# Kernel tuning notes

Hardware: AMD Instinct MI355X
Metric: run time of the kernel (lower is better)

Reference implementation:

```python
import jax, jax.numpy as jnp
import numpy as np

N = 100000
C_IN = 128
HEADS = 4
D_HEAD = 32
E = 1600000
NEG_SLOPE = 0.2
LN_EPS = 1e-5


def setup_inputs() -> dict:
    key = jax.random.key(0)
    ks = jax.random.split(key, 8)
    x = jax.random.normal(ks[0], (N, C_IN), dtype=jnp.float32)
    edge_index = jax.random.randint(ks[1], (2, E), 0, N, dtype=jnp.int32)
    # LayerNorm affine params
    ln_gamma = jnp.ones((C_IN,), jnp.float32)
    ln_beta = jnp.zeros((C_IN,), jnp.float32)
    # GATv2 linear layers (lin_l for source/messages, lin_r for target), glorot-ish scale
    scale = 1.0 / np.sqrt(C_IN)
    W_l = jax.random.normal(ks[2], (C_IN, HEADS * D_HEAD), jnp.float32) * scale
    b_l = jnp.zeros((HEADS * D_HEAD,), jnp.float32)
    W_r = jax.random.normal(ks[3], (C_IN, HEADS * D_HEAD), jnp.float32) * scale
    b_r = jnp.zeros((HEADS * D_HEAD,), jnp.float32)
    att = jax.random.normal(ks[4], (HEADS, D_HEAD), jnp.float32) * (1.0 / np.sqrt(D_HEAD))
    bias = jnp.zeros((D_HEAD,), jnp.float32)  # concat=False -> out_channels bias
    return {"x": x, "edge_index": edge_index, "ln_gamma": ln_gamma, "ln_beta": ln_beta,
            "W_l": W_l, "b_l": b_l, "W_r": W_r, "b_r": b_r, "att": att, "bias": bias}


def reference(x, edge_index, ln_gamma, ln_beta, W_l, b_l, W_r, b_r, att, bias):
    n = x.shape[0]
    # LayerNorm + ReLU (dropout_mask=None / eval mode)
    mu = jnp.mean(x, axis=-1, keepdims=True)
    var = jnp.mean(jnp.square(x - mu), axis=-1, keepdims=True)
    xh = (x - mu) * jax.lax.rsqrt(var + LN_EPS) * ln_gamma + ln_beta
    xh = jax.nn.relu(xh)
    # add self loops
    loops = jnp.arange(n, dtype=edge_index.dtype)
    src = jnp.concatenate([edge_index[0], loops])  # message sources j
    dst = jnp.concatenate([edge_index[1], loops])  # aggregation targets i
    # GATv2: separate transforms for source and target
    x_l = (xh @ W_l + b_l).reshape(n, HEADS, D_HEAD)
    x_r = (xh @ W_r + b_r).reshape(n, HEADS, D_HEAD)
    # edge scores: e_ij = att . leaky_relu(x_l[j] + x_r[i])
    s = x_l[src] + x_r[dst]                                      # [E+N, H, Dh]
    e = jnp.einsum('ehd,hd->eh', jax.nn.leaky_relu(s, NEG_SLOPE), att)
    # segment softmax over destination node
    m = jax.ops.segment_max(e, dst, num_segments=n)              # [N, H]
    w = jnp.exp(e - m[dst])
    denom = jax.ops.segment_sum(w, dst, num_segments=n)          # [N, H]
    alpha = w / (denom[dst] + 1e-16)                             # [E+N, H]
    # scatter-aggregate messages alpha * x_l[j]
    out = jax.ops.segment_sum(alpha[:, :, None] * x_l[src], dst, num_segments=n)  # [N, H, Dh]
    # concat=False -> mean over heads, then bias
    return out.mean(axis=1) + bias
```

## Files before the change

### kernel.cpp

```cpp
#include <hip/hip_runtime.h>
#include <math.h>


typedef __bf16 bf16x8 __attribute__((ext_vector_type(8)));
typedef float f32x4 __attribute__((ext_vector_type(4)));
typedef _Float16 h2 __attribute__((ext_vector_type(2)));

#define BIN_T 4096
#define NB_MAX 1024
#define AST 136
#define HST 136

static __device__ __forceinline__ unsigned short f2bf(float f) {
  union { float f; unsigned u; } v;
  v.f = f;
  const unsigned r = v.u + 0x7fffu + ((v.u >> 16) & 1u);
  return (unsigned short)(r >> 16);
}
static __device__ __forceinline__ float bf2f(unsigned short h) {
  union { float f; unsigned u; } v;
  v.u = ((unsigned)h) << 16;
  return v.f;
}

static __device__ __forceinline__ float quad_reduce_add(float p) {
  int a = __builtin_amdgcn_mov_dpp(__builtin_bit_cast(int, p),
                                   0xB1 , 0xf, 0xf,
                                   true);
  p += __builtin_bit_cast(float, a);
  int b = __builtin_amdgcn_mov_dpp(__builtin_bit_cast(int, p),
                                   0x4E , 0xf, 0xf,
                                   true);
  p += __builtin_bit_cast(float, b);
  return p;
}

__global__ __launch_bounds__(256) void pack_w_k(
    const float* __restrict__ Wl, const float* __restrict__ Wr,
    unsigned short* __restrict__ wph, unsigned short* __restrict__ wpl) {
  const int idx = blockIdx.x * 256 + threadIdx.x;
  const int mat = idx >> 14;
  const int rem = idx & 16383;
  const int k = rem >> 7;
  const int c = rem & 127;
  const float v = (mat ? Wr : Wl)[rem];
  const unsigned short h = f2bf(v);
  const unsigned short lo = f2bf(v - bf2f(h));
  const int po = ((mat * 4 + (k >> 5)) * 128 + c) * 32 + (k & 31);
  wph[po] = h;
  wpl[po] = lo;
}

__global__ __launch_bounds__(512, 5) void ln_gemm_mfma_k(
    const float* __restrict__ x, const float* __restrict__ gamma,
    const float* __restrict__ beta,
    const unsigned short* __restrict__ wph,
    const unsigned short* __restrict__ wpl,
    const float* __restrict__ bl, const float* __restrict__ br,
    _Float16* __restrict__ xl16, _Float16* __restrict__ xr16, int n) {
  __shared__ char smem[64 * AST * 2 * 2];
  unsigned short* const ah = (unsigned short*)smem;
  unsigned short* const al = ah + 64 * AST;
  _Float16* const sth = (_Float16*)smem;

  const int t = threadIdx.x;
  const int blk = blockIdx.x * 64;

  {
    const int r = t >> 3, q = t & 7;
    const int node = blk + r;
    float4 v[4];
    float s = 0.f, s2 = 0.f;
    const float* xrow = x + (size_t)node * 128;
#pragma unroll
    for (int rep = 0; rep < 4; rep++) {
      float4 f = make_float4(0.f, 0.f, 0.f, 0.f);
      if (node < n) f = *(const float4*)(xrow + 4 * q + 32 * rep);
      v[rep] = f;
      s += f.x + f.y + f.z + f.w;
      s2 += f.x * f.x + f.y * f.y + f.z * f.z + f.w * f.w;
    }
    s += __shfl_xor(s, 1);  s += __shfl_xor(s, 2);  s += __shfl_xor(s, 4);
    s2 += __shfl_xor(s2, 1); s2 += __shfl_xor(s2, 2); s2 += __shfl_xor(s2, 4);
    const float mu = s * (1.f / 128.f);
    const float rs = rsqrtf(s2 * (1.f / 128.f) - mu * mu + 1e-5f);
#pragma unroll
    for (int rep = 0; rep < 4; rep++) {
      const int k0 = 4 * q + 32 * rep;
      const float4 g4 = *(const float4*)(gamma + k0);
      const float4 b4 = *(const float4*)(beta + k0);
      const float ev[4] = {v[rep].x, v[rep].y, v[rep].z, v[rep].w};
      const float gv[4] = {g4.x, g4.y, g4.z, g4.w};
      const float bv[4] = {b4.x, b4.y, b4.z, b4.w};
      unsigned short hs[4], ls[4];
#pragma unroll
      for (int i2 = 0; i2 < 4; i2++) {
        float xv = (ev[i2] - mu) * rs * gv[i2] + bv[i2];
        xv = fmaxf(xv, 0.f);
        const unsigned short h = f2bf(xv);
        hs[i2] = h;
        ls[i2] = f2bf(xv - bf2f(h));
      }
      *(ushort4*)(&ah[r * AST + k0]) = make_ushort4(hs[0], hs[1], hs[2], hs[3]);
      *(ushort4*)(&al[r * AST + k0]) = make_ushort4(ls[0], ls[1], ls[2], ls[3]);
    }
  }
  __syncthreads();

  const int lane = t & 63;
  const int w = t >> 6;
  const int mat = w >> 2;
  const int cbase = (w & 3) * 32;
  const int m16 = lane & 15;
  const int quad = lane >> 4;
  const float* const biasp = mat ? br : bl;

  f32x4 acc[2][4];
  float bc[2];
#pragma unroll
  for (int ct = 0; ct < 2; ct++) {
    const int c = cbase + ct * 16 + m16;
    bf16x8 Bh[4], Bl8[4];
#pragma unroll
    for (int kb = 0; kb < 4; kb++) {
      const int bo = ((mat * 4 + kb) * 128 + c) * 32 + quad * 8;
      Bh[kb]  = *(const bf16x8*)(wph + bo);
      Bl8[kb] = *(const bf16x8*)(wpl + bo);
    }
    bc[ct] = biasp[c];
#pragma unroll
    for (int rt = 0; rt < 4; rt++) {
      f32x4 a = {0.f, 0.f, 0.f, 0.f};
#pragma unroll
      for (int kb = 0; kb < 4; kb++) {
        const int ao = (rt * 16 + m16) * AST + kb * 32 + quad * 8;
        const bf16x8 Ah  = *(const bf16x8*)(ah + ao);
        const bf16x8 Al8 = *(const bf16x8*)(al + ao);
        a = __builtin_amdgcn_mfma_f32_16x16x32_bf16(Ah,  Bh[kb],  a, 0, 0, 0);
        a = __builtin_amdgcn_mfma_f32_16x16x32_bf16(Al8, Bh[kb],  a, 0, 0, 0);
        a = __builtin_amdgcn_mfma_f32_16x16x32_bf16(Ah,  Bl8[kb], a, 0, 0, 0);
      }
      acc[ct][rt] = a;
    }
  }

  unsigned short* const outs[2] = {(unsigned short*)xl16,
                                   (unsigned short*)xr16};
#pragma unroll
  for (int round = 0; round < 2; round++) {
    __syncthreads();
    if (mat == 1 - round) {
#pragma unroll
      for (int ct = 0; ct < 2; ct++)
#pragma unroll
        for (int rt = 0; rt < 4; rt++)
#pragma unroll
          for (int g = 0; g < 4; g++)
            sth[(rt * 16 + quad * 4 + g) * HST + cbase + ct * 16 + m16] =
                (_Float16)(acc[ct][rt][g] + bc[ct]);
    }
    __syncthreads();
    unsigned short* const dst = outs[1 - round];
#pragma unroll
    for (int pass = 0; pass < 2; pass++) {
      const int idx = pass * 512 + t;
      const int row = idx >> 4;
      const int c8 = (idx & 15) * 8;
      const int node = blk + row;
      if (node < n)
        *(uint4*)(dst + (size_t)node * 128 + c8) =
            *(const uint4*)((const unsigned short*)sth + row * HST + c8);
    }
  }
}

__global__ __launch_bounds__(256) void hist_lds_k(
    const int* __restrict__ dst_arr, int* __restrict__ bucket_cnt,
    int E, int NB) {
  __shared__ int h[NB_MAX];
  const int t = threadIdx.x;
  for (int b = t; b < NB; b += 256) h[b] = 0;
  __syncthreads();
  const int beg = blockIdx.x * BIN_T;
  const int end = min(beg + BIN_T, E);
  for (int j0 = beg + t * 4; j0 < end; j0 += 1024) {
    if (j0 + 4 <= end) {
      const int4 d4 = *(const int4*)(dst_arr + j0);
      atomicAdd(&h[d4.x >> 7], 1);
      atomicAdd(&h[d4.y >> 7], 1);
      atomicAdd(&h[d4.z >> 7], 1);
      atomicAdd(&h[d4.w >> 7], 1);
    } else {
      for (int j = j0; j < end; j++) atomicAdd(&h[dst_arr[j] >> 7], 1);
    }
  }
  __syncthreads();
  for (int b = t; b < NB; b += 256) {
    const int v = h[b];
    if (v) atomicAdd(&bucket_cnt[b], v);
  }
}

__global__ __launch_bounds__(1024) void bucket_scan_k(
    const int* __restrict__ bucket_cnt, int* __restrict__ bucket_edge_off,
    int* __restrict__ bucket_cur, int* __restrict__ offsets,
    int NB, int N, int M) {
  __shared__ int lds[1024];
  const int t = threadIdx.x;
  const int v = (t < NB) ? bucket_cnt[t] : 0;
  lds[t] = v;
  __syncthreads();
  for (int d = 1; d < 1024; d <<= 1) {
    int u = 0;
    if (t >= d) u = lds[t - d];
    __syncthreads();
    lds[t] += u;
    __syncthreads();
  }
  if (t < NB) {
    const int excl = lds[t] - v;
    bucket_edge_off[t] = excl;
    bucket_cur[t] = excl;
    if (t == NB - 1) bucket_edge_off[NB] = lds[t];
  }
  if (t == 0) offsets[N] = M;
}

__global__ __launch_bounds__(256) void bin2_k(
    const int* __restrict__ ei, int* __restrict__ bucket_cur,
    unsigned* __restrict__ binned, int E, int NB) {
  __shared__ int h[NB_MAX];
  __shared__ int cur[NB_MAX];
  const int t = threadIdx.x;
  for (int b = t; b < NB; b += 256) h[b] = 0;
  __syncthreads();
  const int beg = blockIdx.x * BIN_T;
  const int end = min(beg + BIN_T, E);
  for (int j0 = beg + t * 4; j0 < end; j0 += 1024) {
    if (j0 + 4 <= end) {
      const int4 d4 = *(const int4*)(ei + E + j0);
      atomicAdd(&h[d4.x >> 7], 1);
      atomicAdd(&h[d4.y >> 7], 1);
      atomicAdd(&h[d4.z >> 7], 1);
      atomicAdd(&h[d4.w >> 7], 1);
    } else {
      for (int j = j0; j < end; j++) atomicAdd(&h[ei[E + j] >> 7], 1);
    }
  }
  __syncthreads();
  for (int b = t; b < NB; b += 256) {
    const int v = h[b];
    cur[b] = v ? atomicAdd(&bucket_cur[b], v) : 0;
  }
  __syncthreads();
  for (int j0 = beg + t * 4; j0 < end; j0 += 1024) {
    if (j0 + 4 <= end) {
      const int4 s4 = *(const int4*)(ei + j0);
      const int4 d4 = *(const int4*)(ei + E + j0);
      binned[atomicAdd(&cur[d4.x >> 7], 1)] =
          (((unsigned)d4.x & 127u) << 25) | (unsigned)s4.x;
      binned[atomicAdd(&cur[d4.y >> 7], 1)] =
          (((unsigned)d4.y & 127u) << 25) | (unsigned)s4.y;
      binned[atomicAdd(&cur[d4.z >> 7], 1)] =
          (((unsigned)d4.z & 127u) << 25) | (unsigned)s4.z;
      binned[atomicAdd(&cur[d4.w >> 7], 1)] =
          (((unsigned)d4.w & 127u) << 25) | (unsigned)s4.w;
    } else {
      for (int j = j0; j < end; j++) {
        const int s = ei[j], d = ei[E + j];
        binned[atomicAdd(&cur[d >> 7], 1)] =
            (((unsigned)d & 127u) << 25) | (unsigned)s;
      }
    }
  }
}

__global__ __launch_bounds__(256) void csr_build_k(
    const unsigned* __restrict__ binned,
    const int* __restrict__ bucket_edge_off,
    int* __restrict__ csr_src, int* __restrict__ offsets, int N, int M) {
  __shared__ int s_cnt[128];
  __shared__ int s_off[128];
  __shared__ int s_cur[128];
  const int b = blockIdx.x;
  const int t = threadIdx.x;
  if (b == 0 && t < 16) csr_src[M + t] = 0;
  const int eb = bucket_edge_off[b];
  const int ee = bucket_edge_off[b + 1];
  const int node0 = b << 7;
  if (t < 128) s_cnt[t] = 0;
  __syncthreads();
  for (int j = eb + t; j < ee; j += 256) {
    atomicAdd(&s_cnt[binned[j] >> 25], 1);
  }
  __syncthreads();
  int w = 0;
  if (t < 128) w = (node0 + t < N) ? (s_cnt[t] + 1) : 0;
  if (t < 128) s_off[t] = w;
  __syncthreads();
  for (int d = 1; d < 128; d <<= 1) {
    int u = 0;
    if (t < 128 && t >= d) u = s_off[t - d];
    __syncthreads();
    if (t < 128) s_off[t] += u;
    __syncthreads();
  }
  const int base = eb + node0;
  if (t < 128) {
    const int excl = s_off[t] - w;
    const int node = node0 + t;
    if (node < N) {
      offsets[node] = base + excl;
      csr_src[base + excl] = node;
      s_cur[t] = excl + 1;
    }
  }
  __syncthreads();
  for (int j = eb + t; j < ee; j += 256) {
    const unsigned e = binned[j];
    const int pos = atomicAdd(&s_cur[e >> 25], 1);
    csr_src[base + pos] = (int)(e & 0x1ffffffu);
  }
}

__global__ __launch_bounds__(256) void agg_fused_k(
    const uint4* __restrict__ xl4, const uint4* __restrict__ xr4,
    const float* __restrict__ att, const int* __restrict__ csr_src,
    const int* __restrict__ offsets, const float* __restrict__ bias,
    float* __restrict__ out, int n) {
  const int t = threadIdx.x;
  const int wid = t >> 6;
  const int lane = t & 63;
  const int u = lane & 15;
  const int g = lane >> 4;
  const int nwaves = gridDim.x * 4;

  h2 at[4];
  {
    const float4 a0 = *(const float4*)(att + u * 8);
    const float4 a1 = *(const float4*)(att + u * 8 + 4);
    at[0] = h2{(_Float16)a0.x, (_Float16)a0.y};
    at[1] = h2{(_Float16)a0.z, (_Float16)a0.w};
    at[2] = h2{(_Float16)a1.x, (_Float16)a1.y};
    at[3] = h2{(_Float16)a1.z, (_Float16)a1.w};
  }
  float4 b0, b1;
  if (lane < 4) {
    b0 = *(const float4*)(bias + lane * 8);
    b1 = *(const float4*)(bias + lane * 8 + 4);
  }

  const h2 slope = h2{(_Float16)0.2f, (_Float16)0.2f};
  const char* const xb = (const char*)xl4;
  const unsigned ub = (unsigned)u << 4;
  union U { uint4 u4; h2 h[4]; unsigned ui[4]; };

  for (int i = blockIdx.x * 4 + wid; i < n; i += nwaves) {
    const int off = offsets[i];
    const int end = offsets[i + 1];

    U xru; xru.u4 = xr4[(size_t)i * 16 + u];

    float den = 0.f;
    float acc[8] = {0.f, 0.f, 0.f, 0.f, 0.f, 0.f, 0.f, 0.f};

    uint4 rA = *(const uint4*)(xb + (((unsigned)csr_src[off + g] << 8) + ub));
    uint4 rB =
        *(const uint4*)(xb + (((unsigned)csr_src[off + 4 + g] << 8) + ub));

    for (int jb = off; jb < end; jb += 4) {
      U xv; xv.u4 = rA;
      rA = rB;
      rB = *(const uint4*)(xb + (((unsigned)csr_src[jb + 8 + g] << 8) + ub));

      float p = 0.f;
#pragma unroll
      for (int k = 0; k < 4; k++) {
        const h2 s = xv.h[k] + xru.h[k];
        const h2 l = __builtin_elementwise_max(s, s * slope);
        p = __builtin_amdgcn_fdot2(l, at[k], p, false);
      }
      p = quad_reduce_add(p);

      const float wgt = (jb + g < end) ? __expf(p) : 0.f;
      den += wgt;
#pragma unroll
      for (int k = 0; k < 4; k++) {
        asm("v_fma_mix_f32 %0, %1, %2, %0 op_sel:[0,0,0] op_sel_hi:[0,1,0]"
            : "+v"(acc[2 * k]) : "v"(wgt), "v"(xv.ui[k]));
        asm("v_fma_mix_f32 %0, %1, %2, %0 op_sel:[0,1,0] op_sel_hi:[0,1,0]"
            : "+v"(acc[2 * k + 1]) : "v"(wgt), "v"(xv.ui[k]));
      }
    }

    den += __shfl_xor(den, 16);
    den += __shfl_xor(den, 32);
#pragma unroll
    for (int m = 0; m < 8; m++) {
      acc[m] += __shfl_xor(acc[m], 16);
      acc[m] += __shfl_xor(acc[m], 32);
    }
    const float rd = 1.0f / (den + 1e-16f);
#pragma unroll
    for (int m = 0; m < 8; m++) acc[m] *= rd;
#pragma unroll
    for (int m = 0; m < 8; m++) {
      acc[m] += __shfl_xor(acc[m], 4);
      acc[m] += __shfl_xor(acc[m], 8);
    }
    if (lane < 4) {
      float4 o0 = make_float4(acc[0] * 0.25f + b0.x, acc[1] * 0.25f + b0.y,
                              acc[2] * 0.25f + b0.z, acc[3] * 0.25f + b0.w);
      float4 o1 = make_float4(acc[4] * 0.25f + b1.x, acc[5] * 0.25f + b1.y,
                              acc[6] * 0.25f + b1.z, acc[7] * 0.25f + b1.w);
      *(float4*)(out + (size_t)i * 32 + lane * 8) = o0;
      *(float4*)(out + (size_t)i * 32 + lane * 8 + 4) = o1;
    }
  }
}

extern "C" void kernel_launch(void* const* d_in, const int* in_sizes, int n_in,
                              void* d_out, int out_size, void* d_ws,
                              size_t ws_size, hipStream_t stream) {
  const float* x     = (const float*)d_in[0];
  const int*   ei    = (const int*)d_in[1];
  const float* gamma = (const float*)d_in[2];
  const float* beta  = (const float*)d_in[3];
  const float* Wl    = (const float*)d_in[4];
  const float* bl    = (const float*)d_in[5];
  const float* Wr    = (const float*)d_in[6];
  const float* br    = (const float*)d_in[7];
  const float* att   = (const float*)d_in[8];
  const float* bias  = (const float*)d_in[9];
  float* out = (float*)d_out;

  const int N = in_sizes[0] / 128;
  const int E = in_sizes[1] / 2;
  const int M = E + N;
  const int NB = (N + 127) / 128;

  char* p = (char*)d_ws;
  size_t o = 0;
  auto alloc = [&](size_t bytes) -> void* {
    void* r = (void*)(p + o);
    o = (o + bytes + 255) & ~(size_t)255;
    return r;
  };
  _Float16* xl16   = (_Float16*)alloc((size_t)N * 128 * 2);
  unsigned* binned = (unsigned*)xl16;
  _Float16* xr16 = (_Float16*)alloc((size_t)N * 128 * 2);
  int*   csr_src = (int*)alloc((size_t)M * 4 + 64);
  int*   offsets = (int*)alloc((size_t)(N + 1) * 4);
  int*   bucket_cnt = (int*)alloc((size_t)NB * 4);
  int*   bucket_off = (int*)alloc((size_t)(NB + 1) * 4);
  int*   bucket_cur = (int*)alloc((size_t)NB * 4);
  unsigned short* wph = (unsigned short*)alloc(2 * 128 * 128 * 2);
  unsigned short* wpl = (unsigned short*)alloc(2 * 128 * 128 * 2);
  (void)n_in; (void)out_size; (void)ws_size;

  const int nchunks = (E + BIN_T - 1) / BIN_T;

  hipMemsetAsync(bucket_cnt, 0, (size_t)NB * 4, stream);
  hist_lds_k<<<nchunks, 256, 0, stream>>>(ei + E, bucket_cnt, E, NB);
  bucket_scan_k<<<1, 1024, 0, stream>>>(bucket_cnt, bucket_off, bucket_cur,
                                        offsets, NB, N, M);
  bin2_k<<<nchunks, 256, 0, stream>>>(ei, bucket_cur, binned, E, NB);
  csr_build_k<<<NB, 256, 0, stream>>>(binned, bucket_off, csr_src, offsets,
                                      N, M);

  pack_w_k<<<128, 256, 0, stream>>>(Wl, Wr, wph, wpl);
  ln_gemm_mfma_k<<<(N + 63) / 64, 512, 0, stream>>>(x, gamma, beta, wph, wpl,
                                                    bl, br, xl16, xr16, N);

  const int nodeWaves = (N + 3) / 4;
  const int aggBlocks = nodeWaves < 2048 ? nodeWaves : 2048;
  agg_fused_k<<<aggBlocks, 256, 0, stream>>>((const uint4*)xl16,
                                             (const uint4*)xr16, att,
                                             csr_src, offsets, bias, out, N);
}
```

Measured before the change: 261.3 us.

## Reuse per-chunk histograms in binning, prescale CSR indices, deepen gather prefetch

The histogram kernel now writes each chunk's bucket counts to workspace, so the binning kernel no longer rereads the destination array and rebuilds its LDS histogram. The CSR source indices are stored pre-shifted by the 256-byte row stride, which removes a shift per gathered row in the aggregation loop. The aggregation loop prefetches one extra edge index ahead (three-deep row pipeline), and the attention vector is prescaled by log2(e) so the exponential can use the native exp2 instruction. The cost is extra workspace traffic for the per-chunk histograms and a few more registers for the deeper prefetch.

```diff
diff --git a/kernel.cpp b/kernel.cpp
--- a/kernel.cpp
+++ b/kernel.cpp
@@ -176,7 +176,7 @@
 
 __global__ __launch_bounds__(256) void hist_lds_k(
     const int* __restrict__ dst_arr, int* __restrict__ bucket_cnt,
-    int E, int NB) {
+    int* __restrict__ hist_chunks, int E, int NB) {
   __shared__ int h[NB_MAX];
   const int t = threadIdx.x;
   for (int b = t; b < NB; b += 256) h[b] = 0;
@@ -195,8 +195,10 @@
     }
   }
   __syncthreads();
+  int* const hc = hist_chunks + (size_t)blockIdx.x * NB;
   for (int b = t; b < NB; b += 256) {
     const int v = h[b];
+    hc[b] = v;
     if (v) atomicAdd(&bucket_cnt[b], v);
   }
 }
@@ -228,31 +230,18 @@
 
 __global__ __launch_bounds__(256) void bin2_k(
     const int* __restrict__ ei, int* __restrict__ bucket_cur,
+    const int* __restrict__ hist_chunks,
     unsigned* __restrict__ binned, int E, int NB) {
-  __shared__ int h[NB_MAX];
   __shared__ int cur[NB_MAX];
   const int t = threadIdx.x;
-  for (int b = t; b < NB; b += 256) h[b] = 0;
+  const int* const hc = hist_chunks + (size_t)blockIdx.x * NB;
+  for (int b = t; b < NB; b += 256) {
+    const int v = hc[b];
+    cur[b] = v ? atomicAdd(&bucket_cur[b], v) : 0;
+  }
   __syncthreads();
   const int beg = blockIdx.x * BIN_T;
   const int end = min(beg + BIN_T, E);
-  for (int j0 = beg + t * 4; j0 < end; j0 += 1024) {
-    if (j0 + 4 <= end) {
-      const int4 d4 = *(const int4*)(ei + E + j0);
-      atomicAdd(&h[d4.x >> 7], 1);
-      atomicAdd(&h[d4.y >> 7], 1);
-      atomicAdd(&h[d4.z >> 7], 1);
-      atomicAdd(&h[d4.w >> 7], 1);
-    } else {
-      for (int j = j0; j < end; j++) atomicAdd(&h[ei[E + j] >> 7], 1);
-    }
-  }
-  __syncthreads();
-  for (int b = t; b < NB; b += 256) {
-    const int v = h[b];
-    cur[b] = v ? atomicAdd(&bucket_cur[b], v) : 0;
-  }
-  __syncthreads();
   for (int j0 = beg + t * 4; j0 < end; j0 += 1024) {
     if (j0 + 4 <= end) {
       const int4 s4 = *(const int4*)(ei + j0);
@@ -278,7 +267,7 @@
 __global__ __launch_bounds__(256) void csr_build_k(
     const unsigned* __restrict__ binned,
     const int* __restrict__ bucket_edge_off,
-    int* __restrict__ csr_src, int* __restrict__ offsets, int N, int M) {
+    unsigned* __restrict__ csr_src, int* __restrict__ offsets, int N, int M) {
   __shared__ int s_cnt[128];
   __shared__ int s_off[128];
   __shared__ int s_cur[128];
@@ -311,7 +300,7 @@
     const int node = node0 + t;
     if (node < N) {
       offsets[node] = base + excl;
-      csr_src[base + excl] = node;
+      csr_src[base + excl] = (unsigned)node << 8;
       s_cur[t] = excl + 1;
     }
   }
@@ -319,13 +308,13 @@
   for (int j = eb + t; j < ee; j += 256) {
     const unsigned e = binned[j];
     const int pos = atomicAdd(&s_cur[e >> 25], 1);
-    csr_src[base + pos] = (int)(e & 0x1ffffffu);
+    csr_src[base + pos] = (e & 0x1ffffffu) << 8;
   }
 }
 
 __global__ __launch_bounds__(256) void agg_fused_k(
     const uint4* __restrict__ xl4, const uint4* __restrict__ xr4,
-    const float* __restrict__ att, const int* __restrict__ csr_src,
+    const float* __restrict__ att, const unsigned* __restrict__ csr_src,
     const int* __restrict__ offsets, const float* __restrict__ bias,
     float* __restrict__ out, int n) {
   const int t = threadIdx.x;
@@ -337,12 +326,13 @@
 
   h2 at[4];
   {
+    const float L2E = 1.44269504f;
     const float4 a0 = *(const float4*)(att + u * 8);
     const float4 a1 = *(const float4*)(att + u * 8 + 4);
-    at[0] = h2{(_Float16)a0.x, (_Float16)a0.y};
-    at[1] = h2{(_Float16)a0.z, (_Float16)a0.w};
-    at[2] = h2{(_Float16)a1.x, (_Float16)a1.y};
-    at[3] = h2{(_Float16)a1.z, (_Float16)a1.w};
+    at[0] = h2{(_Float16)(a0.x * L2E), (_Float16)(a0.y * L2E)};
+    at[1] = h2{(_Float16)(a0.z * L2E), (_Float16)(a0.w * L2E)};
+    at[2] = h2{(_Float16)(a1.x * L2E), (_Float16)(a1.y * L2E)};
+    at[3] = h2{(_Float16)(a1.z * L2E), (_Float16)(a1.w * L2E)};
   }
   float4 b0, b1;
   if (lane < 4) {
@@ -351,8 +341,7 @@
   }
 
   const h2 slope = h2{(_Float16)0.2f, (_Float16)0.2f};
-  const char* const xb = (const char*)xl4;
-  const unsigned ub = (unsigned)u << 4;
+  const char* const xbu = (const char*)xl4 + ((unsigned)u << 4);
   union U { uint4 u4; h2 h[4]; unsigned ui[4]; };
 
   for (int i = blockIdx.x * 4 + wid; i < n; i += nwaves) {
@@ -364,14 +353,14 @@
     float den = 0.f;
     float acc[8] = {0.f, 0.f, 0.f, 0.f, 0.f, 0.f, 0.f, 0.f};
 
-    uint4 rA = *(const uint4*)(xb + (((unsigned)csr_src[off + g] << 8) + ub));
-    uint4 rB =
-        *(const uint4*)(xb + (((unsigned)csr_src[off + 4 + g] << 8) + ub));
+    unsigned iC = csr_src[off + 8 + g];
+    uint4 rA = *(const uint4*)(xbu + csr_src[off + g]);
+    uint4 rB = *(const uint4*)(xbu + csr_src[off + 4 + g]);
 
     for (int jb = off; jb < end; jb += 4) {
       U xv; xv.u4 = rA;
-      rA = rB;
-      rB = *(const uint4*)(xb + (((unsigned)csr_src[jb + 8 + g] << 8) + ub));
+      const uint4 rC = *(const uint4*)(xbu + iC);
+      iC = csr_src[jb + 12 + g];
 
       float p = 0.f;
 #pragma unroll
@@ -382,7 +371,8 @@
       }
       p = quad_reduce_add(p);
 
-      const float wgt = (jb + g < end) ? __expf(p) : 0.f;
+      const float wgt =
+          (jb + g < end) ? __builtin_amdgcn_exp2f(p) : 0.f;
       den += wgt;
 #pragma unroll
       for (int k = 0; k < 4; k++) {
@@ -391,6 +381,8 @@
         asm("v_fma_mix_f32 %0, %1, %2, %0 op_sel:[0,1,0] op_sel_hi:[0,1,0]"
             : "+v"(acc[2 * k + 1]) : "v"(wgt), "v"(xv.ui[k]));
       }
+      rA = rB;
+      rB = rC;
     }
 
     den += __shfl_xor(den, 16);
@@ -438,6 +430,7 @@
   const int E = in_sizes[1] / 2;
   const int M = E + N;
   const int NB = (N + 127) / 128;
+  const int nchunks = (E + BIN_T - 1) / BIN_T;
 
   char* p = (char*)d_ws;
   size_t o = 0;
@@ -449,22 +442,23 @@
   _Float16* xl16   = (_Float16*)alloc((size_t)N * 128 * 2);
   unsigned* binned = (unsigned*)xl16;
   _Float16* xr16 = (_Float16*)alloc((size_t)N * 128 * 2);
-  int*   csr_src = (int*)alloc((size_t)M * 4 + 64);
+  unsigned* csr_src = (unsigned*)alloc((size_t)M * 4 + 64);
   int*   offsets = (int*)alloc((size_t)(N + 1) * 4);
   int*   bucket_cnt = (int*)alloc((size_t)NB * 4);
   int*   bucket_off = (int*)alloc((size_t)(NB + 1) * 4);
   int*   bucket_cur = (int*)alloc((size_t)NB * 4);
+  int*   hist_chunks = (int*)alloc((size_t)nchunks * NB * 4);
   unsigned short* wph = (unsigned short*)alloc(2 * 128 * 128 * 2);
   unsigned short* wpl = (unsigned short*)alloc(2 * 128 * 128 * 2);
   (void)n_in; (void)out_size; (void)ws_size;
 
-  const int nchunks = (E + BIN_T - 1) / BIN_T;
-
   hipMemsetAsync(bucket_cnt, 0, (size_t)NB * 4, stream);
-  hist_lds_k<<<nchunks, 256, 0, stream>>>(ei + E, bucket_cnt, E, NB);
+  hist_lds_k<<<nchunks, 256, 0, stream>>>(ei + E, bucket_cnt, hist_chunks,
+                                          E, NB);
   bucket_scan_k<<<1, 1024, 0, stream>>>(bucket_cnt, bucket_off, bucket_cur,
                                         offsets, NB, N, M);
-  bin2_k<<<nchunks, 256, 0, stream>>>(ei, bucket_cur, binned, E, NB);
+  bin2_k<<<nchunks, 256, 0, stream>>>(ei, bucket_cur, hist_chunks, binned,
+                                      E, NB);
   csr_build_k<<<NB, 256, 0, stream>>>(binned, bucket_off, csr_src, offsets,
                                       N, M);
 
```

Measured after the change: 265.6 us. About the same (+1.6%).

## Prefetch next node's CSR data across iterations and pre-shift source offsets

Applied to the files above, without the earlier changes.

The aggregation loop now prefetches the next node's offsets, its x_r row and its first source indices while the current node's reduction runs, so the next node's gather loads are issued before the current epilogue finishes. CSR source indices are stored pre-shifted by 8 (byte offsets), which removes the shift and add from the inner gather. The attention vector is pre-scaled by log2(e) so the native exp2 can replace expf. The trade-offs are more live registers and lower fp16 precision in the scaled attention weights.

```diff
diff --git a/kernel.cpp b/kernel.cpp
--- a/kernel.cpp
+++ b/kernel.cpp
@@ -278,7 +278,7 @@
 __global__ __launch_bounds__(256) void csr_build_k(
     const unsigned* __restrict__ binned,
     const int* __restrict__ bucket_edge_off,
-    int* __restrict__ csr_src, int* __restrict__ offsets, int N, int M) {
+    unsigned* __restrict__ csr_src, int* __restrict__ offsets, int N, int M) {
   __shared__ int s_cnt[128];
   __shared__ int s_off[128];
   __shared__ int s_cur[128];
@@ -311,7 +311,7 @@
     const int node = node0 + t;
     if (node < N) {
       offsets[node] = base + excl;
-      csr_src[base + excl] = node;
+      csr_src[base + excl] = (unsigned)node << 8;
       s_cur[t] = excl + 1;
     }
   }
@@ -319,13 +319,13 @@
   for (int j = eb + t; j < ee; j += 256) {
     const unsigned e = binned[j];
     const int pos = atomicAdd(&s_cur[e >> 25], 1);
-    csr_src[base + pos] = (int)(e & 0x1ffffffu);
+    csr_src[base + pos] = (e & 0x1ffffffu) << 8;
   }
 }
 
 __global__ __launch_bounds__(256) void agg_fused_k(
     const uint4* __restrict__ xl4, const uint4* __restrict__ xr4,
-    const float* __restrict__ att, const int* __restrict__ csr_src,
+    const float* __restrict__ att, const unsigned* __restrict__ csr_src,
     const int* __restrict__ offsets, const float* __restrict__ bias,
     float* __restrict__ out, int n) {
   const int t = threadIdx.x;
@@ -337,12 +337,13 @@
 
   h2 at[4];
   {
+    const float L2E = 1.44269504f;
     const float4 a0 = *(const float4*)(att + u * 8);
     const float4 a1 = *(const float4*)(att + u * 8 + 4);
-    at[0] = h2{(_Float16)a0.x, (_Float16)a0.y};
-    at[1] = h2{(_Float16)a0.z, (_Float16)a0.w};
-    at[2] = h2{(_Float16)a1.x, (_Float16)a1.y};
-    at[3] = h2{(_Float16)a1.z, (_Float16)a1.w};
+    at[0] = h2{(_Float16)(a0.x * L2E), (_Float16)(a0.y * L2E)};
+    at[1] = h2{(_Float16)(a0.z * L2E), (_Float16)(a0.w * L2E)};
+    at[2] = h2{(_Float16)(a1.x * L2E), (_Float16)(a1.y * L2E)};
+    at[3] = h2{(_Float16)(a1.z * L2E), (_Float16)(a1.w * L2E)};
   }
   float4 b0, b1;
   if (lane < 4) {
@@ -351,27 +352,32 @@
   }
 
   const h2 slope = h2{(_Float16)0.2f, (_Float16)0.2f};
-  const char* const xb = (const char*)xl4;
-  const unsigned ub = (unsigned)u << 4;
+  const char* const xbu = (const char*)xl4 + ((unsigned)u << 4);
   union U { uint4 u4; h2 h[4]; unsigned ui[4]; };
 
-  for (int i = blockIdx.x * 4 + wid; i < n; i += nwaves) {
-    const int off = offsets[i];
-    const int end = offsets[i + 1];
-
-    U xru; xru.u4 = xr4[(size_t)i * 16 + u];
+  int i = blockIdx.x * 4 + wid;
+  if (i >= n) return;
+
+  int off = offsets[i];
+  int end = offsets[i + 1];
+  U xru; xru.u4 = xr4[(size_t)i * 16 + u];
+  uint4 rA = *(const uint4*)(xbu + csr_src[off + g]);
+  uint4 rB = *(const uint4*)(xbu + csr_src[off + 4 + g]);
+
+  while (true) {
+    const int inext = i + nwaves;
+    const int isel = (inext < n) ? inext : i;
+    const int offn = offsets[isel];
+    const int endn = offsets[isel + 1];
+    U xrn; xrn.u4 = xr4[(size_t)isel * 16 + u];
 
     float den = 0.f;
     float acc[8] = {0.f, 0.f, 0.f, 0.f, 0.f, 0.f, 0.f, 0.f};
-
-    uint4 rA = *(const uint4*)(xb + (((unsigned)csr_src[off + g] << 8) + ub));
-    uint4 rB =
-        *(const uint4*)(xb + (((unsigned)csr_src[off + 4 + g] << 8) + ub));
 
     for (int jb = off; jb < end; jb += 4) {
       U xv; xv.u4 = rA;
       rA = rB;
-      rB = *(const uint4*)(xb + (((unsigned)csr_src[jb + 8 + g] << 8) + ub));
+      rB = *(const uint4*)(xbu + csr_src[jb + 8 + g]);
 
       float p = 0.f;
 #pragma unroll
@@ -382,7 +388,7 @@
       }
       p = quad_reduce_add(p);
 
-      const float wgt = (jb + g < end) ? __expf(p) : 0.f;
+      const float wgt = (jb + g < end) ? __builtin_amdgcn_exp2f(p) : 0.f;
       den += wgt;
 #pragma unroll
       for (int k = 0; k < 4; k++) {
@@ -392,6 +398,9 @@
             : "+v"(acc[2 * k + 1]) : "v"(wgt), "v"(xv.ui[k]));
       }
     }
+
+    const unsigned niA = csr_src[offn + g];
+    const unsigned niB = csr_src[offn + 4 + g];
 
     den += __shfl_xor(den, 16);
     den += __shfl_xor(den, 32);
@@ -416,6 +425,14 @@
       *(float4*)(out + (size_t)i * 32 + lane * 8) = o0;
       *(float4*)(out + (size_t)i * 32 + lane * 8 + 4) = o1;
     }
+
+    if (inext >= n) break;
+    i = inext;
+    off = offn;
+    end = endn;
+    xru = xrn;
+    rA = *(const uint4*)(xbu + niA);
+    rB = *(const uint4*)(xbu + niB);
   }
 }
 
@@ -438,6 +455,7 @@
   const int E = in_sizes[1] / 2;
   const int M = E + N;
   const int NB = (N + 127) / 128;
+  const int nchunks = (E + BIN_T - 1) / BIN_T;
 
   char* p = (char*)d_ws;
   size_t o = 0;
@@ -449,7 +467,7 @@
   _Float16* xl16   = (_Float16*)alloc((size_t)N * 128 * 2);
   unsigned* binned = (unsigned*)xl16;
   _Float16* xr16 = (_Float16*)alloc((size_t)N * 128 * 2);
-  int*   csr_src = (int*)alloc((size_t)M * 4 + 64);
+  unsigned* csr_src = (unsigned*)alloc((size_t)M * 4 + 64);
   int*   offsets = (int*)alloc((size_t)(N + 1) * 4);
   int*   bucket_cnt = (int*)alloc((size_t)NB * 4);
   int*   bucket_off = (int*)alloc((size_t)(NB + 1) * 4);
@@ -458,8 +476,6 @@
   unsigned short* wpl = (unsigned short*)alloc(2 * 128 * 128 * 2);
   (void)n_in; (void)out_size; (void)ws_size;
 
-  const int nchunks = (E + BIN_T - 1) / BIN_T;
-
   hipMemsetAsync(bucket_cnt, 0, (size_t)NB * 4, stream);
   hist_lds_k<<<nchunks, 256, 0, stream>>>(ei + E, bucket_cnt, E, NB);
   bucket_scan_k<<<1, 1024, 0, stream>>>(bucket_cnt, bucket_off, bucket_cur,
```

Measured after the change: 257.6 us. Within noise of the previous version (-1.4%).
